# Kernel optimization log

Hardware: AMD Instinct MI355X
Metric: run time of the kernel (lower is better)

Reference implementation:

```python
import jax, jax.numpy as jnp
import numpy as np

B, T, D_IN, D_OUT = 4, 2048, 1024, 1024


def setup_inputs() -> dict:
    key = jax.random.key(0)
    k1, k2, k3, k4 = jax.random.split(key, 4)
    s = 0.02  # keep activations in a sane range
    x = jax.random.normal(k1, (B, T, D_IN), dtype=jnp.float32)
    Wq = jax.random.normal(k2, (D_IN, D_OUT), dtype=jnp.float32) * s
    Wk = jax.random.normal(k3, (D_IN, D_OUT), dtype=jnp.float32) * s
    Wv = jax.random.normal(k4, (D_IN, D_OUT), dtype=jnp.float32) * s
    return {"x": x, "Wq": Wq, "Wk": Wk, "Wv": Wv}


def reference(x, Wq, Wk, Wv):
    # Linear projections (torch Linear: y = x @ W^T, here W stored as [d_in, d_out])
    q = jnp.einsum('btd,de->bte', x, Wq)
    k = jnp.einsum('btd,de,->bte', x, Wk, jnp.float32(1.0)) if False else jnp.einsum('btd,de->bte', x, Wk)
    v = jnp.einsum('btd,de->bte', x, Wv)
    # Full [B, T, T] score matrix (faithful to the hand-rolled implementation)
    scores = jnp.einsum('bqe,bke->bqk', q, k)
    T_ = x.shape[1]
    causal = jnp.triu(jnp.ones((T_, T_), dtype=bool), k=1)  # True above diagonal
    scores = jnp.where(causal[None, :, :], -jnp.inf, scores)
    scale = 1.0 / jnp.sqrt(jnp.asarray(k.shape[-1], dtype=scores.dtype))
    attn = jax.nn.softmax(scores * scale, axis=-1)
    # dropout p=0.0 -> identity
    return jnp.einsum('bqk,bke->bqe', attn, v)
```

## Files before the change

### kernel.cpp

```cpp
#include <hip/hip_runtime.h>
#include <hip/hip_bf16.h>
#include <cstdint>

typedef __attribute__((ext_vector_type(8))) short short8;
typedef __attribute__((ext_vector_type(4))) short short4v;
typedef __attribute__((ext_vector_type(4))) float floatx4;
typedef unsigned short ushort;

__device__ __forceinline__ float bf2f(ushort u) {
  unsigned int x = ((unsigned int)u) << 16;
  return __builtin_bit_cast(float, x);
}
__device__ __forceinline__ ushort f2bf(float f) {
  unsigned int x = __builtin_bit_cast(unsigned int, f);
  x += 0x7fffu + ((x >> 16) & 1u);
  return (ushort)(x >> 16);
}

__device__ __forceinline__ void gload_lds16(const void* g, void* l) {
  __builtin_amdgcn_global_load_lds(
      (const __attribute__((address_space(1))) void*)g,
      (__attribute__((address_space(3))) void*)l, 16, 0, 0);
}


__global__ __launch_bounds__(256) void cvtx_kernel(const float* __restrict__ x,
                                                   ushort* __restrict__ xb) {
  int i = blockIdx.x * 256 + threadIdx.x;
  const float4* xf = (const float4*)x;
  float4 a = xf[i * 2], b = xf[i * 2 + 1];
  short8 o;
  o[0] = (short)f2bf(a.x); o[1] = (short)f2bf(a.y);
  o[2] = (short)f2bf(a.z); o[3] = (short)f2bf(a.w);
  o[4] = (short)f2bf(b.x); o[5] = (short)f2bf(b.y);
  o[6] = (short)f2bf(b.z); o[7] = (short)f2bf(b.w);
  ((short8*)xb)[i] = o;
}

__global__ __launch_bounds__(256) void wt_kernel(const float* __restrict__ Wq,
                                                 const float* __restrict__ Wk,
                                                 const float* __restrict__ Wv,
                                                 ushort* __restrict__ Wt) {
  int z = blockIdx.z;
  const float* W = z == 0 ? Wq : (z == 1 ? Wk : Wv);
  ushort* O = Wt + (size_t)z * 1024 * 1024;
  __shared__ float tile[64][65];
  int c0 = blockIdx.x * 64;
  int r0 = blockIdx.y * 64;
  int tid = threadIdx.x;
#pragma unroll
  for (int i = 0; i < 4; ++i) {
    int c = tid + i * 256; int rr = c >> 4, q = c & 15;
    float4 v = *(const float4*)&W[(size_t)(r0 + rr) * 1024 + c0 + q * 4];
    tile[rr][q * 4 + 0] = v.x; tile[rr][q * 4 + 1] = v.y;
    tile[rr][q * 4 + 2] = v.z; tile[rr][q * 4 + 3] = v.w;
  }
  __syncthreads();
#pragma unroll
  for (int i = 0; i < 2; ++i) {
    int c = tid + i * 256; int oc = c >> 3, q = c & 7;
    short8 o;
#pragma unroll
    for (int j = 0; j < 8; ++j) o[j] = (short)f2bf(tile[q * 8 + j][oc]);
    *(short8*)&O[(size_t)(c0 + oc) * 1024 + r0 + q * 8] = o;
  }
}


__global__ __launch_bounds__(256, 2) void qkv2_kernel(const ushort* __restrict__ A,
                                                      const ushort* __restrict__ Bm,
                                                      ushort* __restrict__ Qo,
                                                      ushort* __restrict__ Ko,
                                                      ushort* __restrict__ Vt) {
  __shared__ __align__(16) ushort ldsA[3][128 * 32];
  __shared__ __align__(16) ushort ldsB[3][256 * 32];

  const int tid = threadIdx.x;
  const int lane = tid & 63;
  const int wave = tid >> 6;
  const int r15 = lane & 15;
  const int kg = lane >> 4;

  int orig = blockIdx.y * 64 + blockIdx.x;
  int swz = (orig & 7) * 96 + (orig >> 3);
  int bx = swz / 12;
  int by = swz % 12;
  const int m0 = bx * 128;
  const int n0 = by * 256;

  const ushort* Ag = A + (size_t)m0 * 1024;
  const ushort* Bg = Bm + (size_t)n0 * 1024;

  const int NKT = 32;

  floatx4 acc[8][4] = {};

  auto stage = [&](int kt, int slot) {
    int k0 = kt * 32;
#pragma unroll
    for (int i = 0; i < 2; ++i) {
      int c = tid + i * 256;
      int d = c * 16;
      int L = d ^ (((d >> 7) & 3) << 4);
      gload_lds16(Ag + (size_t)(L >> 6) * 1024 + k0 + ((L & 63) >> 1),
                  &ldsA[slot][c * 8]);
    }
#pragma unroll
    for (int i = 0; i < 4; ++i) {
      int c = tid + i * 256;
      int d = c * 16;
      int L = d ^ (((d >> 7) & 3) << 4);
      gload_lds16(Bg + (size_t)(L >> 6) * 1024 + k0 + ((L & 63) >> 1),
                  &ldsB[slot][c * 8]);
    }
  };

  auto ldA = [&](int slot, int m) -> short8 {
    int row = m * 16 + r15;
    int P = (row * 64 + kg * 16) ^ (((row >> 1) & 3) << 4);
    return *(const short8*)((const char*)&ldsA[slot][0] + P);
  };
  auto ldB = [&](int slot, int n) -> short8 {
    int row = wave * 64 + n * 16 + r15;
    int P = (row * 64 + kg * 16) ^ (((row >> 1) & 3) << 4);
    return *(const short8*)((const char*)&ldsB[slot][0] + P);
  };

  stage(0, 0);
  stage(1, 1);
  asm volatile("s_waitcnt vmcnt(6)" ::: "memory");
  __builtin_amdgcn_s_barrier();

  int cur = 0;
  for (int kt = 0; kt < NKT; ++kt) {
    short8 bfrag[4], afrag[4];
#pragma unroll
    for (int n = 0; n < 4; ++n) bfrag[n] = ldB(cur, n);
#pragma unroll
    for (int m = 0; m < 4; ++m) afrag[m] = ldA(cur, m);
    if (kt + 2 < NKT) {
      int slot = cur + 2; if (slot >= 3) slot -= 3;
      stage(kt + 2, slot);
    }
    __builtin_amdgcn_s_barrier();
    asm volatile("s_waitcnt lgkmcnt(0)" ::: "memory");
    __builtin_amdgcn_sched_barrier(0);
    __builtin_amdgcn_s_setprio(1);
#pragma unroll
    for (int m = 0; m < 4; ++m)
#pragma unroll
      for (int n = 0; n < 4; ++n)
        acc[m][n] = __builtin_amdgcn_mfma_f32_16x16x32_bf16(afrag[m], bfrag[n], acc[m][n], 0, 0, 0);
    __builtin_amdgcn_s_setprio(0);
    __builtin_amdgcn_s_barrier();

#pragma unroll
    for (int m = 0; m < 4; ++m) afrag[m] = ldA(cur, m + 4);
    if (kt >= NKT - 3) {
      asm volatile("s_waitcnt vmcnt(0)" ::: "memory");
    } else {
      asm volatile("s_waitcnt vmcnt(6)" ::: "memory");
    }
    __builtin_amdgcn_s_barrier();
    asm volatile("s_waitcnt lgkmcnt(0)" ::: "memory");
    __builtin_amdgcn_sched_barrier(0);
    __builtin_amdgcn_s_setprio(1);
#pragma unroll
    for (int m = 0; m < 4; ++m)
#pragma unroll
      for (int n = 0; n < 4; ++n)
        acc[m + 4][n] = __builtin_amdgcn_mfma_f32_16x16x32_bf16(afrag[m], bfrag[n], acc[m + 4][n], 0, 0, 0);
    __builtin_amdgcn_s_setprio(0);
    __builtin_amdgcn_s_barrier();

    ++cur; if (cur >= 3) cur = 0;
  }

  const int z = n0 >> 10;
  const int rq = kg * 4;
  if (z < 2) {
    ushort* Cz = z == 0 ? Qo : Ko;
    const int cb = n0 & 1023;
#pragma unroll
    for (int m = 0; m < 8; ++m) {
#pragma unroll
      for (int n = 0; n < 4; ++n) {
        int gc = cb + wave * 64 + n * 16 + r15;
#pragma unroll
        for (int r = 0; r < 4; ++r) {
          int gr = m0 + m * 16 + rq + r;
          Cz[(size_t)gr * 1024 + gc] = f2bf(acc[m][n][r]);
        }
      }
    }
  } else {
#pragma unroll
    for (int m = 0; m < 8; ++m) {
      int gr = m0 + m * 16 + rq;
      int b = gr >> 11;
      int t = gr & 2047;
      ushort* Vb = Vt + (size_t)b * 1024 * 2048;
#pragma unroll
      for (int n = 0; n < 4; ++n) {
        int e = (n0 - 2048) + wave * 64 + n * 16 + r15;
        short4v o;
#pragma unroll
        for (int r = 0; r < 4; ++r) o[r] = (short)f2bf(acc[m][n][r]);
        *(short4v*)&Vb[(size_t)e * 2048 + t] = o;
      }
    }
  }
}


template <bool OUT_BF16>
__device__ __forceinline__ void gemm_tn_core(const ushort* __restrict__ A,
                                             const ushort* __restrict__ B,
                                             void* __restrict__ C,
                                             int lda, int ldb, int ldc,
                                             int m0, int n0, int kTiles) {
  __shared__ __align__(16) ushort Asm[2][128 * 32];
  __shared__ __align__(16) ushort Bsm[2][128 * 32];
  const int tid = threadIdx.x;
  const int lane = tid & 63;
  const int wave = tid >> 6;
  const int wrow = (wave >> 1) * 64;
  const int wcol = (wave & 1) * 64;
  const int r15 = lane & 15;
  const int kg = (lane >> 4) * 8;

  floatx4 acc[4][4] = {};

  const ushort* Ag = A + (size_t)m0 * lda;
  const ushort* Bg = B + (size_t)n0 * ldb;

  auto stage = [&](int buf, int kt) {
    int k0 = kt * 32;
#pragma unroll
    for (int i = 0; i < 2; ++i) {
      int c = tid + i * 256;
      gload_lds16(Ag + (size_t)(c >> 2) * lda + k0 + (c & 3) * 8, &Asm[buf][c * 8]);
    }
#pragma unroll
    for (int i = 0; i < 2; ++i) {
      int c = tid + i * 256;
      gload_lds16(Bg + (size_t)(c >> 2) * ldb + k0 + (c & 3) * 8, &Bsm[buf][c * 8]);
    }
  };

  stage(0, 0);
  for (int kt = 0; kt < kTiles; ++kt) {
    int cur = kt & 1;
    __syncthreads();
    if (kt + 1 < kTiles) stage(cur ^ 1, kt + 1);
    const ushort* As = Asm[cur];
    const ushort* Bs = Bsm[cur];
    short8 af[4], bfr[4];
#pragma unroll
    for (int m = 0; m < 4; ++m)
      af[m] = *(const short8*)&As[(wrow + m * 16 + r15) * 32 + kg];
#pragma unroll
    for (int n = 0; n < 4; ++n)
      bfr[n] = *(const short8*)&Bs[(wcol + n * 16 + r15) * 32 + kg];
#pragma unroll
    for (int m = 0; m < 4; ++m)
#pragma unroll
      for (int n = 0; n < 4; ++n)
        acc[m][n] = __builtin_amdgcn_mfma_f32_16x16x32_bf16(af[m], bfr[n], acc[m][n], 0, 0, 0);
  }

  const int rq = (lane >> 4) * 4;
#pragma unroll
  for (int m = 0; m < 4; ++m) {
#pragma unroll
    for (int n = 0; n < 4; ++n) {
      int gc = n0 + wcol + n * 16 + r15;
#pragma unroll
      for (int r = 0; r < 4; ++r) {
        int gr = m0 + wrow + m * 16 + rq + r;
        if (OUT_BF16)
          ((ushort*)C)[(size_t)gr * ldc + gc] = f2bf(acc[m][n][r]);
        else
          ((float*)C)[(size_t)gr * ldc + gc] = acc[m][n][r];
      }
    }
  }
}

__global__ __launch_bounds__(256) void s_kernel(const ushort* __restrict__ Q,
                                                const ushort* __restrict__ K,
                                                ushort* __restrict__ S) {
  int t = blockIdx.x;
  int qb = (int)((sqrtf(8.f * (float)t + 1.f) - 1.f) * 0.5f);
  while ((qb + 1) * (qb + 2) / 2 <= t) ++qb;
  while (qb * (qb + 1) / 2 > t) --qb;
  int kb = t - qb * (qb + 1) / 2;
  size_t b = blockIdx.y;
  gemm_tn_core<true>(Q + b * 2048 * 1024, K + b * 2048 * 1024, S + b * 2048 * 2048,
                     1024, 1024, 2048, qb * 128, kb * 128, 32);
}

__global__ __launch_bounds__(256) void pv_kernel(const ushort* __restrict__ P,
                                                 const ushort* __restrict__ Vt,
                                                 float* __restrict__ O) {
  int qb = blockIdx.x;
  size_t b = blockIdx.z;
  gemm_tn_core<false>(P + b * 2048 * 2048, Vt + b * 1024 * 2048, O + b * 2048 * 1024,
                      2048, 2048, 1024, qb * 128, blockIdx.y * 128, (qb + 1) * 4);
}

__global__ __launch_bounds__(256) void softmax_kernel(ushort* __restrict__ S) {
  const int r = blockIdx.x;
  const int b = blockIdx.y;
  ushort* row = S + ((size_t)b * 2048 + r) * 2048;
  const int len = r + 1;
  const int padEnd = ((r >> 7) + 1) << 7;
  const int tid = threadIdx.x;
  const int base = tid * 8;
  const float scale = 0.03125f;

  float v[8];
  float mymax = -1e30f;
  if (base < len) {
    short8 s = *(const short8*)(row + base);
#pragma unroll
    for (int j = 0; j < 8; ++j) {
      float f = (base + j < len) ? bf2f((ushort)s[j]) : -1e30f;
      v[j] = f;
      mymax = fmaxf(mymax, f);
    }
  } else {
#pragma unroll
    for (int j = 0; j < 8; ++j) v[j] = -1e30f;
  }

  __shared__ float redm[4], reds[4];
  const int wave = tid >> 6, lane = tid & 63;
#pragma unroll
  for (int off = 32; off > 0; off >>= 1) mymax = fmaxf(mymax, __shfl_xor(mymax, off, 64));
  if (lane == 0) redm[wave] = mymax;
  __syncthreads();
  float m = fmaxf(fmaxf(redm[0], redm[1]), fmaxf(redm[2], redm[3])) * scale;

  float p[8];
  float mysum = 0.f;
#pragma unroll
  for (int j = 0; j < 8; ++j) {
    float e = (base + j < len) ? __expf(v[j] * scale - m) : 0.f;
    p[j] = e;
    mysum += e;
  }
#pragma unroll
  for (int off = 32; off > 0; off >>= 1) mysum += __shfl_xor(mysum, off, 64);
  if (lane == 0) reds[wave] = mysum;
  __syncthreads();
  float inv = 1.f / (reds[0] + reds[1] + reds[2] + reds[3]);

  if (base < padEnd) {
    short8 o;
#pragma unroll
    for (int j = 0; j < 8; ++j) o[j] = (short)f2bf(p[j] * inv);
    *(short8*)(row + base) = o;
  }
}


extern "C" void kernel_launch(void* const* d_in, const int* in_sizes, int n_in,
                              void* d_out, int out_size, void* d_ws, size_t ws_size,
                              hipStream_t stream) {
  const float* x  = (const float*)d_in[0];
  const float* Wq = (const float*)d_in[1];
  const float* Wk = (const float*)d_in[2];
  const float* Wv = (const float*)d_in[3];
  float* out = (float*)d_out;

  ushort* Xb  = (ushort*)d_ws;
  ushort* Wt  = Xb + (size_t)8192 * 1024;
  ushort* QK  = Wt + (size_t)3 * 1024 * 1024;
  ushort* Vt  = QK + (size_t)2 * 8192 * 1024;
  ushort* S   = Vt + (size_t)4 * 1024 * 2048;

  ushort* Qp = QK;
  ushort* Kp = QK + (size_t)8192 * 1024;

  hipLaunchKernelGGL(cvtx_kernel, dim3(4096), dim3(256), 0, stream, x, Xb);
  hipLaunchKernelGGL(wt_kernel, dim3(16, 16, 3), dim3(256), 0, stream, Wq, Wk, Wv, Wt);
  hipLaunchKernelGGL(qkv2_kernel, dim3(64, 12), dim3(256), 0, stream, Xb, Wt, Qp, Kp, Vt);
  hipLaunchKernelGGL(s_kernel, dim3(136, 4), dim3(256), 0, stream, Qp, Kp, S);
  hipLaunchKernelGGL(softmax_kernel, dim3(2048, 4), dim3(256), 0, stream, S);
  hipLaunchKernelGGL(pv_kernel, dim3(16, 8, 4), dim3(256), 0, stream, S, Vt, out);
}
```

Baseline: 187.3 us.

## Merge prep kernels, retile QKV GEMM, split softmax into stats plus fused PV

```diff
diff --git a/kernel.cpp b/kernel.cpp
--- a/kernel.cpp
+++ b/kernel.cpp
@@ -24,201 +24,202 @@
 }
 
 
-__global__ __launch_bounds__(256) void cvtx_kernel(const float* __restrict__ x,
-                                                   ushort* __restrict__ xb) {
-  int i = blockIdx.x * 256 + threadIdx.x;
-  const float4* xf = (const float4*)x;
-  float4 a = xf[i * 2], b = xf[i * 2 + 1];
-  short8 o;
-  o[0] = (short)f2bf(a.x); o[1] = (short)f2bf(a.y);
-  o[2] = (short)f2bf(a.z); o[3] = (short)f2bf(a.w);
-  o[4] = (short)f2bf(b.x); o[5] = (short)f2bf(b.y);
-  o[6] = (short)f2bf(b.z); o[7] = (short)f2bf(b.w);
-  ((short8*)xb)[i] = o;
-}
-
-__global__ __launch_bounds__(256) void wt_kernel(const float* __restrict__ Wq,
-                                                 const float* __restrict__ Wk,
-                                                 const float* __restrict__ Wv,
-                                                 ushort* __restrict__ Wt) {
-  int z = blockIdx.z;
-  const float* W = z == 0 ? Wq : (z == 1 ? Wk : Wv);
-  ushort* O = Wt + (size_t)z * 1024 * 1024;
-  __shared__ float tile[64][65];
-  int c0 = blockIdx.x * 64;
-  int r0 = blockIdx.y * 64;
+__global__ __launch_bounds__(256) void prep_kernel(const float* __restrict__ x,
+                                                   const float* __restrict__ Wq,
+                                                   const float* __restrict__ Wk,
+                                                   const float* __restrict__ Wv,
+                                                   ushort* __restrict__ xb,
+                                                   ushort* __restrict__ Wt) {
+  int bid = blockIdx.x;
   int tid = threadIdx.x;
-#pragma unroll
-  for (int i = 0; i < 4; ++i) {
-    int c = tid + i * 256; int rr = c >> 4, q = c & 15;
-    float4 v = *(const float4*)&W[(size_t)(r0 + rr) * 1024 + c0 + q * 4];
-    tile[rr][q * 4 + 0] = v.x; tile[rr][q * 4 + 1] = v.y;
-    tile[rr][q * 4 + 2] = v.z; tile[rr][q * 4 + 3] = v.w;
-  }
-  __syncthreads();
-#pragma unroll
-  for (int i = 0; i < 2; ++i) {
-    int c = tid + i * 256; int oc = c >> 3, q = c & 7;
+  if (bid < 4096) {
+    int i = bid * 256 + tid;
+    const float4* xf = (const float4*)x;
+    float4 a = xf[i * 2], b = xf[i * 2 + 1];
     short8 o;
-#pragma unroll
-    for (int j = 0; j < 8; ++j) o[j] = (short)f2bf(tile[q * 8 + j][oc]);
-    *(short8*)&O[(size_t)(c0 + oc) * 1024 + r0 + q * 8] = o;
-  }
-}
-
-
-__global__ __launch_bounds__(256, 2) void qkv2_kernel(const ushort* __restrict__ A,
+    o[0] = (short)f2bf(a.x); o[1] = (short)f2bf(a.y);
+    o[2] = (short)f2bf(a.z); o[3] = (short)f2bf(a.w);
+    o[4] = (short)f2bf(b.x); o[5] = (short)f2bf(b.y);
+    o[6] = (short)f2bf(b.z); o[7] = (short)f2bf(b.w);
+    ((short8*)xb)[i] = o;
+  } else {
+    int t = bid - 4096;
+    int z = t >> 8;
+    int rem = t & 255;
+    int c0 = (rem & 15) * 64;
+    int r0 = (rem >> 4) * 64;
+    const float* W = z == 0 ? Wq : (z == 1 ? Wk : Wv);
+    ushort* O = Wt + (size_t)z * 1024 * 1024;
+    __shared__ float tile[64][65];
+#pragma unroll
+    for (int i = 0; i < 4; ++i) {
+      int c = tid + i * 256; int rr = c >> 4, q = c & 15;
+      float4 v = *(const float4*)&W[(size_t)(r0 + rr) * 1024 + c0 + q * 4];
+      tile[rr][q * 4 + 0] = v.x; tile[rr][q * 4 + 1] = v.y;
+      tile[rr][q * 4 + 2] = v.z; tile[rr][q * 4 + 3] = v.w;
+    }
+    __syncthreads();
+#pragma unroll
+    for (int i = 0; i < 2; ++i) {
+      int c = tid + i * 256; int oc = c >> 3, q = c & 7;
+      short8 o;
+#pragma unroll
+      for (int j = 0; j < 8; ++j) o[j] = (short)f2bf(tile[q * 8 + j][oc]);
+      *(short8*)&O[(size_t)(c0 + oc) * 1024 + r0 + q * 8] = o;
+    }
+  }
+}
+
+
+__global__ __launch_bounds__(512, 2) void qkv8_kernel(const ushort* __restrict__ A,
                                                       const ushort* __restrict__ Bm,
                                                       ushort* __restrict__ Qo,
                                                       ushort* __restrict__ Ko,
                                                       ushort* __restrict__ Vt) {
-  __shared__ __align__(16) ushort ldsA[3][128 * 32];
-  __shared__ __align__(16) ushort ldsB[3][256 * 32];
+  __shared__ __align__(16) ushort ldsA[2][2][8192];
+  __shared__ __align__(16) ushort ldsB[2][2][6144];
 
   const int tid = threadIdx.x;
   const int lane = tid & 63;
   const int wave = tid >> 6;
+  const int wm = wave >> 2;
+  const int wn = wave & 3;
   const int r15 = lane & 15;
   const int kg = lane >> 4;
 
-  int orig = blockIdx.y * 64 + blockIdx.x;
-  int swz = (orig & 7) * 96 + (orig >> 3);
-  int bx = swz / 12;
-  int by = swz % 12;
-  const int m0 = bx * 128;
-  const int n0 = by * 256;
+  int orig = blockIdx.y * 32 + blockIdx.x;
+  int swz = (orig & 7) * 64 + (orig >> 3);
+  const int m0 = (swz >> 4) * 256;
+  const int n0 = (swz & 15) * 192;
 
   const ushort* Ag = A + (size_t)m0 * 1024;
   const ushort* Bg = Bm + (size_t)n0 * 1024;
 
-  const int NKT = 32;
-
-  floatx4 acc[8][4] = {};
-
-  auto stage = [&](int kt, int slot) {
-    int k0 = kt * 32;
-#pragma unroll
-    for (int i = 0; i < 2; ++i) {
-      int c = tid + i * 256;
-      int d = c * 16;
-      int L = d ^ (((d >> 7) & 3) << 4);
-      gload_lds16(Ag + (size_t)(L >> 6) * 1024 + k0 + ((L & 63) >> 1),
-                  &ldsA[slot][c * 8]);
-    }
-#pragma unroll
-    for (int i = 0; i < 4; ++i) {
-      int c = tid + i * 256;
-      int d = c * 16;
-      int L = d ^ (((d >> 7) & 3) << 4);
-      gload_lds16(Bg + (size_t)(L >> 6) * 1024 + k0 + ((L & 63) >> 1),
-                  &ldsB[slot][c * 8]);
-    }
-  };
-
-  auto ldA = [&](int slot, int m) -> short8 {
-    int row = m * 16 + r15;
+  const int NKT = 16;
+
+  floatx4 acc[8][3] = {};
+
+  auto stage = [&](int s) {
+    const int j = s >> 2, hh = s & 3;
+    const int isA = !(hh & 1);
+    const int kh = hh >> 1;
+    const int kbase = j * 64 + kh * 32;
+    if (isA) {
+      ushort* dst = &ldsA[j & 1][kh][0];
+#pragma unroll
+      for (int i = 0; i < 2; ++i) {
+        int c = tid + i * 512;
+        int d = c * 16;
+        int L = d ^ (((d >> 7) & 3) << 4);
+        gload_lds16(Ag + (size_t)(L >> 6) * 1024 + kbase + ((L & 63) >> 1), dst + c * 8);
+      }
+    } else {
+      ushort* dst = &ldsB[j & 1][kh][0];
+#pragma unroll
+      for (int i = 0; i < 2; ++i) {
+        int c = tid + i * 512;
+        if (c < 768) {
+          int d = c * 16;
+          int L = d ^ (((d >> 7) & 3) << 4);
+          gload_lds16(Bg + (size_t)(L >> 6) * 1024 + kbase + ((L & 63) >> 1), dst + c * 8);
+        }
+      }
+    }
+  };
+
+  auto ldA = [&](int buf, int kh, int m) -> short8 {
+    int row = wm * 128 + m * 16 + r15;
     int P = (row * 64 + kg * 16) ^ (((row >> 1) & 3) << 4);
-    return *(const short8*)((const char*)&ldsA[slot][0] + P);
-  };
-  auto ldB = [&](int slot, int n) -> short8 {
-    int row = wave * 64 + n * 16 + r15;
+    return *(const short8*)((const char*)&ldsA[buf][kh][0] + P);
+  };
+  auto ldB = [&](int buf, int kh, int n) -> short8 {
+    int row = wn * 48 + n * 16 + r15;
     int P = (row * 64 + kg * 16) ^ (((row >> 1) & 3) << 4);
-    return *(const short8*)((const char*)&ldsB[slot][0] + P);
-  };
-
-  stage(0, 0);
-  stage(1, 1);
+    return *(const short8*)((const char*)&ldsB[buf][kh][0] + P);
+  };
+
+#pragma unroll
+  for (int s = 0; s < 6; ++s) stage(s);
   asm volatile("s_waitcnt vmcnt(6)" ::: "memory");
   __builtin_amdgcn_s_barrier();
 
-  int cur = 0;
+  short8 bfrag[3], afrag[4];
   for (int kt = 0; kt < NKT; ++kt) {
-    short8 bfrag[4], afrag[4];
-#pragma unroll
-    for (int n = 0; n < 4; ++n) bfrag[n] = ldB(cur, n);
-#pragma unroll
-    for (int m = 0; m < 4; ++m) afrag[m] = ldA(cur, m);
-    if (kt + 2 < NKT) {
-      int slot = cur + 2; if (slot >= 3) slot -= 3;
-      stage(kt + 2, slot);
-    }
-    __builtin_amdgcn_s_barrier();
-    asm volatile("s_waitcnt lgkmcnt(0)" ::: "memory");
-    __builtin_amdgcn_sched_barrier(0);
-    __builtin_amdgcn_s_setprio(1);
-#pragma unroll
-    for (int m = 0; m < 4; ++m)
-#pragma unroll
-      for (int n = 0; n < 4; ++n)
-        acc[m][n] = __builtin_amdgcn_mfma_f32_16x16x32_bf16(afrag[m], bfrag[n], acc[m][n], 0, 0, 0);
-    __builtin_amdgcn_s_setprio(0);
-    __builtin_amdgcn_s_barrier();
-
-#pragma unroll
-    for (int m = 0; m < 4; ++m) afrag[m] = ldA(cur, m + 4);
-    if (kt >= NKT - 3) {
-      asm volatile("s_waitcnt vmcnt(0)" ::: "memory");
-    } else {
-      asm volatile("s_waitcnt vmcnt(6)" ::: "memory");
-    }
-    __builtin_amdgcn_s_barrier();
-    asm volatile("s_waitcnt lgkmcnt(0)" ::: "memory");
-    __builtin_amdgcn_sched_barrier(0);
-    __builtin_amdgcn_s_setprio(1);
-#pragma unroll
-    for (int m = 0; m < 4; ++m)
-#pragma unroll
-      for (int n = 0; n < 4; ++n)
-        acc[m + 4][n] = __builtin_amdgcn_mfma_f32_16x16x32_bf16(afrag[m], bfrag[n], acc[m + 4][n], 0, 0, 0);
-    __builtin_amdgcn_s_setprio(0);
-    __builtin_amdgcn_s_barrier();
-
-    ++cur; if (cur >= 3) cur = 0;
-  }
-
-  const int z = n0 >> 10;
+    const int buf = kt & 1;
+#pragma unroll
+    for (int q = 0; q < 4; ++q) {
+      const int kh = q >> 1;
+      const int msub = (q & 1) * 4;
+      if ((q & 1) == 0) {
+#pragma unroll
+        for (int n = 0; n < 3; ++n) bfrag[n] = ldB(buf, kh, n);
+      }
+#pragma unroll
+      for (int m = 0; m < 4; ++m) afrag[m] = ldA(buf, kh, msub + m);
+      int sidx = kt * 4 + q + 6;
+      if (sidx < NKT * 4) stage(sidx);
+      if (q & 1) {
+        if (kt == NKT - 2 && q == 3)
+          asm volatile("s_waitcnt vmcnt(0)" ::: "memory");
+        else
+          asm volatile("s_waitcnt vmcnt(4)" ::: "memory");
+      }
+      __builtin_amdgcn_s_barrier();
+      asm volatile("s_waitcnt lgkmcnt(0)" ::: "memory");
+      __builtin_amdgcn_sched_barrier(0);
+      __builtin_amdgcn_s_setprio(1);
+#pragma unroll
+      for (int m = 0; m < 4; ++m)
+#pragma unroll
+        for (int n = 0; n < 3; ++n)
+          acc[msub + m][n] =
+              __builtin_amdgcn_mfma_f32_16x16x32_bf16(afrag[m], bfrag[n], acc[msub + m][n], 0, 0, 0);
+      __builtin_amdgcn_s_setprio(0);
+      __builtin_amdgcn_s_barrier();
+    }
+  }
+
   const int rq = kg * 4;
-  if (z < 2) {
-    ushort* Cz = z == 0 ? Qo : Ko;
-    const int cb = n0 & 1023;
-#pragma unroll
-    for (int m = 0; m < 8; ++m) {
-#pragma unroll
-      for (int n = 0; n < 4; ++n) {
-        int gc = cb + wave * 64 + n * 16 + r15;
-#pragma unroll
-        for (int r = 0; r < 4; ++r) {
-          int gr = m0 + m * 16 + rq + r;
-          Cz[(size_t)gr * 1024 + gc] = f2bf(acc[m][n][r]);
-        }
+#pragma unroll
+  for (int m = 0; m < 8; ++m) {
+    int grb = m0 + wm * 128 + m * 16 + rq;
+#pragma unroll
+    for (int n = 0; n < 3; ++n) {
+      int gc0 = n0 + wn * 48 + n * 16;
+      if (gc0 < 2048) {
+        ushort* Cz = gc0 < 1024 ? Qo : Ko;
+        int col = (gc0 & 1023) + r15;
+#pragma unroll
+        for (int r = 0; r < 4; ++r)
+          Cz[(size_t)(grb + r) * 1024 + col] = f2bf(acc[m][n][r]);
+      } else {
+        int e = gc0 - 2048 + r15;
+        int b = grb >> 11;
+        int t = grb & 2047;
+        short4v o;
+#pragma unroll
+        for (int r = 0; r < 4; ++r) o[r] = (short)f2bf(acc[m][n][r]);
+        *(short4v*)&Vt[((size_t)b * 1024 + e) * 2048 + t] = o;
       }
     }
-  } else {
-#pragma unroll
-    for (int m = 0; m < 8; ++m) {
-      int gr = m0 + m * 16 + rq;
-      int b = gr >> 11;
-      int t = gr & 2047;
-      ushort* Vb = Vt + (size_t)b * 1024 * 2048;
-#pragma unroll
-      for (int n = 0; n < 4; ++n) {
-        int e = (n0 - 2048) + wave * 64 + n * 16 + r15;
-        short4v o;
-#pragma unroll
-        for (int r = 0; r < 4; ++r) o[r] = (short)f2bf(acc[m][n][r]);
-        *(short4v*)&Vb[(size_t)e * 2048 + t] = o;
-      }
-    }
-  }
-}
-
-
-template <bool OUT_BF16>
-__device__ __forceinline__ void gemm_tn_core(const ushort* __restrict__ A,
-                                             const ushort* __restrict__ B,
-                                             void* __restrict__ C,
-                                             int lda, int ldb, int ldc,
-                                             int m0, int n0, int kTiles) {
+  }
+}
+
+
+__global__ __launch_bounds__(256) void s_kernel(const ushort* __restrict__ Q,
+                                                const ushort* __restrict__ K,
+                                                ushort* __restrict__ S) {
+  int t = blockIdx.x;
+  int qb = (int)((sqrtf(8.f * (float)t + 1.f) - 1.f) * 0.5f);
+  while ((qb + 1) * (qb + 2) / 2 <= t) ++qb;
+  while (qb * (qb + 1) / 2 > t) --qb;
+  int kb = t - qb * (qb + 1) / 2;
+  size_t b = blockIdx.y;
+  const ushort* A = Q + b * 2048 * 1024;
+  const ushort* B = K + b * 2048 * 1024;
+  ushort* C = S + b * 2048 * 2048;
+  const int m0 = qb * 128, n0 = kb * 128;
+
   __shared__ __align__(16) ushort Asm[2][128 * 32];
   __shared__ __align__(16) ushort Bsm[2][128 * 32];
   const int tid = threadIdx.x;
@@ -230,138 +231,189 @@
   const int kg = (lane >> 4) * 8;
 
   floatx4 acc[4][4] = {};
-
-  const ushort* Ag = A + (size_t)m0 * lda;
-  const ushort* Bg = B + (size_t)n0 * ldb;
+  const ushort* Ag = A + (size_t)m0 * 1024;
+  const ushort* Bg = B + (size_t)n0 * 1024;
 
   auto stage = [&](int buf, int kt) {
     int k0 = kt * 32;
 #pragma unroll
     for (int i = 0; i < 2; ++i) {
       int c = tid + i * 256;
-      gload_lds16(Ag + (size_t)(c >> 2) * lda + k0 + (c & 3) * 8, &Asm[buf][c * 8]);
+      gload_lds16(Ag + (size_t)(c >> 2) * 1024 + k0 + (c & 3) * 8, &Asm[buf][c * 8]);
     }
 #pragma unroll
     for (int i = 0; i < 2; ++i) {
       int c = tid + i * 256;
-      gload_lds16(Bg + (size_t)(c >> 2) * ldb + k0 + (c & 3) * 8, &Bsm[buf][c * 8]);
+      gload_lds16(Bg + (size_t)(c >> 2) * 1024 + k0 + (c & 3) * 8, &Bsm[buf][c * 8]);
     }
   };
 
   stage(0, 0);
+  for (int kt = 0; kt < 32; ++kt) {
+    int cur = kt & 1;
+    __syncthreads();
+    if (kt + 1 < 32) stage(cur ^ 1, kt + 1);
+    short8 af[4], bfr[4];
+#pragma unroll
+    for (int m = 0; m < 4; ++m)
+      af[m] = *(const short8*)&Asm[cur][(wrow + m * 16 + r15) * 32 + kg];
+#pragma unroll
+    for (int n = 0; n < 4; ++n)
+      bfr[n] = *(const short8*)&Bsm[cur][(wcol + n * 16 + r15) * 32 + kg];
+#pragma unroll
+    for (int m = 0; m < 4; ++m)
+#pragma unroll
+      for (int n = 0; n < 4; ++n)
+        acc[m][n] = __builtin_amdgcn_mfma_f32_16x16x32_bf16(af[m], bfr[n], acc[m][n], 0, 0, 0);
+  }
+
+  const int rq = (lane >> 4) * 4;
+#pragma unroll
+  for (int m = 0; m < 4; ++m)
+#pragma unroll
+    for (int n = 0; n < 4; ++n) {
+      int gc = n0 + wcol + n * 16 + r15;
+#pragma unroll
+      for (int r = 0; r < 4; ++r)
+        C[(size_t)(m0 + wrow + m * 16 + rq + r) * 2048 + gc] = f2bf(acc[m][n][r]);
+    }
+}
+
+
+__global__ __launch_bounds__(256) void stats_kernel(const ushort* __restrict__ S,
+                                                    float* __restrict__ Mp,
+                                                    float* __restrict__ Lp) {
+  const int row = blockIdx.x * 4 + (threadIdx.x >> 6);
+  const int lane = threadIdx.x & 63;
+  const int b = row >> 11, r = row & 2047;
+  const ushort* rp = S + ((size_t)b * 2048 + r) * 2048;
+  const float K2 = 0.03125f * 1.44269504f;
+
+  float v[32];
+  float mx = -1e30f;
+#pragma unroll
+  for (int c = 0; c < 4; ++c) {
+    short8 s = *(const short8*)(rp + c * 512 + lane * 8);
+#pragma unroll
+    for (int j = 0; j < 8; ++j) {
+      int col = c * 512 + lane * 8 + j;
+      float f = (col <= r) ? bf2f((ushort)s[j]) : -1e30f;
+      v[c * 8 + j] = f;
+      mx = fmaxf(mx, f);
+    }
+  }
+#pragma unroll
+  for (int off = 32; off > 0; off >>= 1) mx = fmaxf(mx, __shfl_xor(mx, off, 64));
+  float m2 = mx * K2;
+  float sum = 0.f;
+#pragma unroll
+  for (int i = 0; i < 32; ++i) sum += __builtin_amdgcn_exp2f(v[i] * K2 - m2);
+#pragma unroll
+  for (int off = 32; off > 0; off >>= 1) sum += __shfl_xor(sum, off, 64);
+  if (lane == 0) {
+    Mp[row] = m2;
+    Lp[row] = 1.f / sum;
+  }
+}
+
+
+__global__ __launch_bounds__(256) void pv_kernel(const ushort* __restrict__ S,
+                                                 const ushort* __restrict__ Vt,
+                                                 const float* __restrict__ Mp,
+                                                 const float* __restrict__ Lp,
+                                                 float* __restrict__ O) {
+  const int qb = blockIdx.x;
+  const int nb = blockIdx.y;
+  const size_t b = blockIdx.z;
+  const int kTiles = (qb + 1) * 4;
+  const ushort* Sb = S + b * 2048 * 2048;
+  const ushort* Vb = Vt + b * 1024 * 2048;
+  float* Ob = O + b * 2048 * 1024;
+
+  __shared__ __align__(16) ushort Asm[2][128 * 32];
+  __shared__ __align__(16) ushort Bsm[2][128 * 32];
+  const int tid = threadIdx.x;
+  const int lane = tid & 63;
+  const int wave = tid >> 6;
+  const int wrow = (wave >> 1) * 64;
+  const int wcol = (wave & 1) * 64;
+  const int r15 = lane & 15;
+  const int kgB = (lane >> 4) * 8;
+
+  const int arow = tid >> 1;
+  const int koff = (tid & 1) * 16;
+  const int gr = qb * 128 + arow;
+  const float Mv = Mp[b * 2048 + gr];
+  const float Lv = Lp[b * 2048 + gr];
+  const float K2 = 0.03125f * 1.44269504f;
+
+  floatx4 acc[4][4] = {};
+
+  auto stageB = [&](int buf, int kt) {
+    int k0 = kt * 32;
+#pragma unroll
+    for (int i = 0; i < 2; ++i) {
+      int c = tid + i * 256;
+      gload_lds16(Vb + (size_t)(nb * 128 + (c >> 2)) * 2048 + k0 + (c & 3) * 8,
+                  &Bsm[buf][c * 8]);
+    }
+  };
+  auto stageA = [&](int buf, int kt) {
+    int k0 = kt * 32 + koff;
+    short8 s0 = *(const short8*)&Sb[(size_t)gr * 2048 + k0];
+    short8 s1 = *(const short8*)&Sb[(size_t)gr * 2048 + k0 + 8];
+    short8 p0, p1;
+#pragma unroll
+    for (int j = 0; j < 8; ++j) {
+      float e0 = (k0 + j <= gr) ? __builtin_amdgcn_exp2f(bf2f((ushort)s0[j]) * K2 - Mv) * Lv : 0.f;
+      float e1 = (k0 + 8 + j <= gr) ? __builtin_amdgcn_exp2f(bf2f((ushort)s1[j]) * K2 - Mv) * Lv : 0.f;
+      p0[j] = (short)f2bf(e0);
+      p1[j] = (short)f2bf(e1);
+    }
+    int base = arow * 64 + koff * 2;
+    int sw = ((arow >> 1) & 3) << 4;
+    *(short8*)((char*)&Asm[buf][0] + (base ^ sw)) = p0;
+    *(short8*)((char*)&Asm[buf][0] + ((base + 16) ^ sw)) = p1;
+  };
+  auto ldA = [&](int buf, int m) -> short8 {
+    int row = wrow + m * 16 + r15;
+    int P = (row * 64 + (lane >> 4) * 16) ^ (((row >> 1) & 3) << 4);
+    return *(const short8*)((const char*)&Asm[buf][0] + P);
+  };
+
+  stageB(0, 0);
+  stageA(0, 0);
+  __syncthreads();
   for (int kt = 0; kt < kTiles; ++kt) {
     int cur = kt & 1;
-    __syncthreads();
-    if (kt + 1 < kTiles) stage(cur ^ 1, kt + 1);
-    const ushort* As = Asm[cur];
-    const ushort* Bs = Bsm[cur];
+    if (kt + 1 < kTiles) {
+      stageB(cur ^ 1, kt + 1);
+      stageA(cur ^ 1, kt + 1);
+    }
     short8 af[4], bfr[4];
 #pragma unroll
-    for (int m = 0; m < 4; ++m)
-      af[m] = *(const short8*)&As[(wrow + m * 16 + r15) * 32 + kg];
+    for (int m = 0; m < 4; ++m) af[m] = ldA(cur, m);
 #pragma unroll
     for (int n = 0; n < 4; ++n)
-      bfr[n] = *(const short8*)&Bs[(wcol + n * 16 + r15) * 32 + kg];
+      bfr[n] = *(const short8*)&Bsm[cur][(wcol + n * 16 + r15) * 32 + kgB];
 #pragma unroll
     for (int m = 0; m < 4; ++m)
 #pragma unroll
       for (int n = 0; n < 4; ++n)
         acc[m][n] = __builtin_amdgcn_mfma_f32_16x16x32_bf16(af[m], bfr[n], acc[m][n], 0, 0, 0);
+    __syncthreads();
   }
 
   const int rq = (lane >> 4) * 4;
 #pragma unroll
-  for (int m = 0; m < 4; ++m) {
+  for (int m = 0; m < 4; ++m)
 #pragma unroll
     for (int n = 0; n < 4; ++n) {
-      int gc = n0 + wcol + n * 16 + r15;
-#pragma unroll
-      for (int r = 0; r < 4; ++r) {
-        int gr = m0 + wrow + m * 16 + rq + r;
-        if (OUT_BF16)
-          ((ushort*)C)[(size_t)gr * ldc + gc] = f2bf(acc[m][n][r]);
-        else
-          ((float*)C)[(size_t)gr * ldc + gc] = acc[m][n][r];
-      }
-    }
-  }
-}
-
-__global__ __launch_bounds__(256) void s_kernel(const ushort* __restrict__ Q,
-                                                const ushort* __restrict__ K,
-                                                ushort* __restrict__ S) {
-  int t = blockIdx.x;
-  int qb = (int)((sqrtf(8.f * (float)t + 1.f) - 1.f) * 0.5f);
-  while ((qb + 1) * (qb + 2) / 2 <= t) ++qb;
-  while (qb * (qb + 1) / 2 > t) --qb;
-  int kb = t - qb * (qb + 1) / 2;
-  size_t b = blockIdx.y;
-  gemm_tn_core<true>(Q + b * 2048 * 1024, K + b * 2048 * 1024, S + b * 2048 * 2048,
-                     1024, 1024, 2048, qb * 128, kb * 128, 32);
-}
-
-__global__ __launch_bounds__(256) void pv_kernel(const ushort* __restrict__ P,
-                                                 const ushort* __restrict__ Vt,
-                                                 float* __restrict__ O) {
-  int qb = blockIdx.x;
-  size_t b = blockIdx.z;
-  gemm_tn_core<false>(P + b * 2048 * 2048, Vt + b * 1024 * 2048, O + b * 2048 * 1024,
-                      2048, 2048, 1024, qb * 128, blockIdx.y * 128, (qb + 1) * 4);
-}
-
-__global__ __launch_bounds__(256) void softmax_kernel(ushort* __restrict__ S) {
-  const int r = blockIdx.x;
-  const int b = blockIdx.y;
-  ushort* row = S + ((size_t)b * 2048 + r) * 2048;
-  const int len = r + 1;
-  const int padEnd = ((r >> 7) + 1) << 7;
-  const int tid = threadIdx.x;
-  const int base = tid * 8;
-  const float scale = 0.03125f;
-
-  float v[8];
-  float mymax = -1e30f;
-  if (base < len) {
-    short8 s = *(const short8*)(row + base);
-#pragma unroll
-    for (int j = 0; j < 8; ++j) {
-      float f = (base + j < len) ? bf2f((ushort)s[j]) : -1e30f;
-      v[j] = f;
-      mymax = fmaxf(mymax, f);
-    }
-  } else {
-#pragma unroll
-    for (int j = 0; j < 8; ++j) v[j] = -1e30f;
-  }
-
-  __shared__ float redm[4], reds[4];
-  const int wave = tid >> 6, lane = tid & 63;
-#pragma unroll
-  for (int off = 32; off > 0; off >>= 1) mymax = fmaxf(mymax, __shfl_xor(mymax, off, 64));
-  if (lane == 0) redm[wave] = mymax;
-  __syncthreads();
-  float m = fmaxf(fmaxf(redm[0], redm[1]), fmaxf(redm[2], redm[3])) * scale;
-
-  float p[8];
-  float mysum = 0.f;
-#pragma unroll
-  for (int j = 0; j < 8; ++j) {
-    float e = (base + j < len) ? __expf(v[j] * scale - m) : 0.f;
-    p[j] = e;
-    mysum += e;
-  }
-#pragma unroll
-  for (int off = 32; off > 0; off >>= 1) mysum += __shfl_xor(mysum, off, 64);
-  if (lane == 0) reds[wave] = mysum;
-  __syncthreads();
-  float inv = 1.f / (reds[0] + reds[1] + reds[2] + reds[3]);
-
-  if (base < padEnd) {
-    short8 o;
-#pragma unroll
-    for (int j = 0; j < 8; ++j) o[j] = (short)f2bf(p[j] * inv);
-    *(short8*)(row + base) = o;
-  }
+      int gc = nb * 128 + wcol + n * 16 + r15;
+#pragma unroll
+      for (int r = 0; r < 4; ++r)
+        Ob[(size_t)(qb * 128 + wrow + m * 16 + rq + r) * 1024 + gc] = acc[m][n][r];
+    }
 }
 
 
@@ -379,14 +431,15 @@
   ushort* QK  = Wt + (size_t)3 * 1024 * 1024;
   ushort* Vt  = QK + (size_t)2 * 8192 * 1024;
   ushort* S   = Vt + (size_t)4 * 1024 * 2048;
+  float*  Mp  = (float*)(S + (size_t)4 * 2048 * 2048);
+  float*  Lp  = Mp + 8192;
 
   ushort* Qp = QK;
   ushort* Kp = QK + (size_t)8192 * 1024;
 
-  hipLaunchKernelGGL(cvtx_kernel, dim3(4096), dim3(256), 0, stream, x, Xb);
-  hipLaunchKernelGGL(wt_kernel, dim3(16, 16, 3), dim3(256), 0, stream, Wq, Wk, Wv, Wt);
-  hipLaunchKernelGGL(qkv2_kernel, dim3(64, 12), dim3(256), 0, stream, Xb, Wt, Qp, Kp, Vt);
+  hipLaunchKernelGGL(prep_kernel, dim3(4864), dim3(256), 0, stream, x, Wq, Wk, Wv, Xb, Wt);
+  hipLaunchKernelGGL(qkv8_kernel, dim3(32, 16), dim3(512), 0, stream, Xb, Wt, Qp, Kp, Vt);
   hipLaunchKernelGGL(s_kernel, dim3(136, 4), dim3(256), 0, stream, Qp, Kp, S);
-  hipLaunchKernelGGL(softmax_kernel, dim3(2048, 4), dim3(256), 0, stream, S);
-  hipLaunchKernelGGL(pv_kernel, dim3(16, 8, 4), dim3(256), 0, stream, S, Vt, out);
-}
+  hipLaunchKernelGGL(stats_kernel, dim3(2048), dim3(256), 0, stream, S, Mp, Lp);
+  hipLaunchKernelGGL(pv_kernel, dim3(16, 8, 4), dim3(256), 0, stream, S, Vt, Mp, Lp, out);
+}
```

After: 199.3 us. +6.4%, slower.
